# Optimization experiments

Measured on AMD Instinct MI355X. Metric: run time of the kernel, lower is better.

Reference implementation:

```python
import jax, jax.numpy as jnp
import numpy as np

N_NODES = 10000
N_EDGES = 640000
IN_CH, HID, OUT_CH = 128, 128, 64


def _gcn_conv(x, edge_index, edge_weight, W, b, n_nodes):
    # PyG GCNConv (default add_self_loops=True, normalize=True, bias=True):
    #   A_hat = A + I ; D = rowsum(A_hat) ; norm_e = D^-1/2[src] * w_e * D^-1/2[dst]
    #   out[dst] += norm_e * (x @ W)[src] ; out += b
    src, dst = edge_index[0], edge_index[1]
    loop = jnp.arange(n_nodes, dtype=edge_index.dtype)
    src = jnp.concatenate([src, loop])
    dst = jnp.concatenate([dst, loop])
    w = jnp.concatenate([edge_weight, jnp.ones((n_nodes,), edge_weight.dtype)])
    deg = jax.ops.segment_sum(w, dst, num_segments=n_nodes)  # scatter on col
    dinv = jnp.where(deg > 0, jax.lax.rsqrt(deg), 0.0).astype(x.dtype)
    norm = dinv[src] * w * dinv[dst]  # [E+N]
    xw = x @ W  # dense GEMM [N, out]
    msg = norm[:, None] * xw[src]  # gather + scale [E+N, out]
    out = jax.ops.segment_sum(msg, dst, num_segments=n_nodes)  # scatter-add
    return out + b


def setup_inputs() -> dict:
    key = jax.random.key(0)
    ks = jax.random.split(key, 8)
    x = jax.random.normal(ks[0], (N_NODES, IN_CH), dtype=jnp.float32)
    edge_index = jax.random.randint(ks[1], (2, N_EDGES), 0, N_NODES, dtype=jnp.int64)
    edge_weight = jax.random.uniform(ks[2], (N_EDGES,), dtype=jnp.float32)
    W1 = jax.random.normal(ks[3], (IN_CH, HID), dtype=jnp.float32) * 0.05
    b1 = jnp.zeros((HID,), jnp.float32)
    W2 = jax.random.normal(ks[4], (HID, OUT_CH), dtype=jnp.float32) * 0.05
    b2 = jnp.zeros((OUT_CH,), jnp.float32)
    return {"x": x, "edge_index": edge_index, "edge_weight": edge_weight,
            "W1": W1, "b1": b1, "W2": W2, "b2": b2}


def reference(x, edge_index, edge_weight, W1, b1, W2, b2):
    h = _gcn_conv(x, edge_index, edge_weight, W1, b1, N_NODES)
    h = jax.nn.relu(h)
    out = _gcn_conv(h, edge_index, edge_weight, W2, b2, N_NODES)
    return out
```

## Files before the change

kernel.cpp:

```cpp
#include <hip/hip_runtime.h>
#include <math.h>

#define N_NODES 10000
#define N_EDGES 640000
#define ELLW    192

#define CHUNKS  64
#define CHUNK_E 10000
#define GB      313

typedef unsigned long long ull;
typedef unsigned int uint;
typedef unsigned short ushort;
typedef unsigned char uchar;

#define FIXED_SCALE 262144.0f


__device__ __forceinline__ float bf_lo(uint u) { return __uint_as_float(u << 16); }
__device__ __forceinline__ float bf_hi(uint u) { return __uint_as_float(u & 0xffff0000u); }
__device__ __forceinline__ ushort f2bf(float v) {
    uint u = __float_as_uint(v);
    uint r = u + 0x7fffu + ((u >> 16) & 1u);
    return (ushort)(r >> 16);
}

__global__ __launch_bounds__(256) void kernelA(const int* __restrict__ ei,
                                               const float* __restrict__ ew,
                                               uint* __restrict__ sd32,
                                               uint* __restrict__ blockcnt,
                                               const float* __restrict__ x,
                                               const float* __restrict__ W1,
                                               ushort* __restrict__ xw1b) {
    __shared__ uint smem[N_NODES];
    const int tid = threadIdx.x;
    if (blockIdx.x < CHUNKS) {
        const int c = blockIdx.x;
        __shared__ int sflag;
        if (tid == 0) sflag = 0;
        for (int i = tid; i < N_NODES; i += 256) smem[i] = 0u;
        __syncthreads();
        int a = (tid < 64) ? ei[2 * (c * CHUNK_E + tid) + 1] : 0;
        if (a) atomicOr(&sflag, 1);
        __syncthreads();
        const int f = sflag;
        const ull* ei64 = (const ull*)ei;
        for (int k = tid; k < CHUNK_E; k += 256) {
            int e = c * CHUNK_E + k;
            int s, d;
            if (f) { s = ei[e];        d = ei[N_EDGES + e]; }
            else   { s = (int)ei64[e]; d = (int)ei64[N_EDGES + e]; }
            float w = ew[e];
            uint fx = (uint)(w * FIXED_SCALE + 0.5f);
            uint old = atomicAdd(&smem[d], (1u << 24) | fx);
            uint r = (old >> 24) & 15u;
            sd32[e] = (r << 28) | ((uint)d << 14) | (uint)s;
        }
        __syncthreads();
        for (int i = tid; i < N_NODES; i += 256)
            blockcnt[c * N_NODES + i] = smem[i];
    } else {
        constexpr int K = 128, TM = 32, KT = 32, NCOL = 128, RPT = 16;
        float* sA = (float*)smem;
        float* sB = sA + TM * (KT + 1);
        int blk = blockIdx.x - CHUNKS;
        int c = tid % NCOL, rr = tid / NCOL;
        int row0 = blk * TM;
        float acc[RPT];
#pragma unroll
        for (int r = 0; r < RPT; ++r) acc[r] = 0.0f;
        for (int k0 = 0; k0 < K; k0 += KT) {
            for (int i = tid; i < TM * KT; i += 256) {
                int r = i / KT, k = i % KT;
                int gr = row0 + r;
                sA[r * (KT + 1) + k] = (gr < N_NODES) ? x[gr * K + k0 + k] : 0.0f;
            }
            for (int i = tid; i < KT * NCOL; i += 256) {
                int k = i / NCOL, cc = i % NCOL;
                sB[k * NCOL + cc] = W1[(k0 + k) * NCOL + cc];
            }
            __syncthreads();
#pragma unroll
            for (int k = 0; k < KT; ++k) {
                float b = sB[k * NCOL + c];
#pragma unroll
                for (int r = 0; r < RPT; ++r)
                    acc[r] += sA[(rr * RPT + r) * (KT + 1) + k] * b;
            }
            __syncthreads();
        }
#pragma unroll
        for (int r = 0; r < RPT; ++r) {
            int gr = row0 + rr * RPT + r;
            if (gr < N_NODES) xw1b[gr * NCOL + c] = f2bf(acc[r]);
        }
    }
}

__global__ __launch_bounds__(256) void scanB(const uint* __restrict__ blockcnt,
                                             uchar* __restrict__ base8,
                                             int* __restrict__ cnt_arr,
                                             float* __restrict__ dinv) {
    int n = blockIdx.x * 256 + threadIdx.x;
    if (n >= N_NODES) return;
    uint wsum = 0;
    int run = 0;
#pragma unroll 8
    for (int c = 0; c < CHUNKS; ++c) {
        uint v = blockcnt[c * N_NODES + n];
        base8[c * N_NODES + n] = (uchar)run;
        run += (int)(v >> 24);
        wsum += v & 0xffffffu;
    }
    cnt_arr[n] = run;
    float dg = 1.0f + (float)wsum * (1.0f / FIXED_SCALE);
    dinv[n] = (float)(1.0 / sqrt((double)dg));
}

__global__ __launch_bounds__(256) void fillC(const uint* __restrict__ sd32,
                                             const float* __restrict__ ew,
                                             const uchar* __restrict__ base8,
                                             const float* __restrict__ dinv,
                                             ull* __restrict__ epack) {
    const int gid = blockIdx.x * 256 + threadIdx.x;
    const int stride = gridDim.x * 256;
    for (int e = gid; e < N_EDGES; e += stride) {
        uint sd = sd32[e];
        int s = (int)(sd & 0x3fffu);
        int d = (int)((sd >> 14) & 0x3fffu);
        int r = (int)(sd >> 28);
        int c = e / CHUNK_E;
        float nrm = dinv[s] * ew[e] * dinv[d];
        int slot = (int)base8[c * N_NODES + d] + r;
        if (slot < ELLW)
            epack[d * ELLW + slot] = ((ull)__float_as_uint(nrm) << 32) | (ull)(uint)s;
    }
}

__global__ __launch_bounds__(256) void aggC(const ushort* __restrict__ xw1b,
                                            const ull* __restrict__ epack,
                                            const int* __restrict__ cnt_arr,
                                            const float* __restrict__ dinv,
                                            const float* __restrict__ b1,
                                            const float* __restrict__ W2,
                                            ushort* __restrict__ xw2b) {
    __shared__ float hl[4][128];
    __shared__ float w2s[128 * 64];
    const uint* __restrict__ xw32 = (const uint*)xw1b;
    const int tid = threadIdx.x;
    int l = tid & 63;
    int wv = tid >> 6;
    int node = blockIdx.x * 4 + wv;

    for (int i = tid; i < 128 * 64; i += 256) w2s[i] = W2[i];

    int cnt = __builtin_amdgcn_readfirstlane(cnt_arr[node]);
    if (cnt > ELLW) cnt = ELLW;
    float dn = dinv[node];
    float d2 = dn * dn;
    uint su = xw32[node * 64 + l];
    float acc0 = d2 * bf_lo(su);
    float acc1 = d2 * bf_hi(su);
    const ull* ep = epack + (long)node * ELLW;
#pragma unroll 8
    for (int j = 0; j < cnt; ++j) {
        ull v = ep[j];
        uint s = (uint)v;
        float n = __uint_as_float((uint)(v >> 32));
        uint u = xw32[s * 64 + l];
        acc0 = fmaf(n, bf_lo(u), acc0);
        acc1 = fmaf(n, bf_hi(u), acc1);
    }
    float2 bb = ((const float2*)b1)[l];
    hl[wv][2 * l]     = fmaxf(acc0 + bb.x, 0.0f);
    hl[wv][2 * l + 1] = fmaxf(acc1 + bb.y, 0.0f);
    __syncthreads();

    float acc = 0.0f;
#pragma unroll 8
    for (int k = 0; k < 128; ++k)
        acc = fmaf(hl[wv][k], w2s[k * 64 + l], acc);
    xw2b[node * 64 + l] = f2bf(acc);
}

__global__ __launch_bounds__(256) void agg2(const ushort* __restrict__ xw2b,
                                            const ull* __restrict__ epack,
                                            const int* __restrict__ cnt_arr,
                                            const float* __restrict__ dinv,
                                            const float* __restrict__ b2,
                                            float* __restrict__ out) {
    const uint* __restrict__ xw32 = (const uint*)xw2b;
    int lane = threadIdx.x & 63;
    int half = lane >> 5;
    int q = lane & 31;
    int pair = blockIdx.x * 4 + (threadIdx.x >> 6);
    int A = pair * 2, B = A + 1;
    int cntA = __builtin_amdgcn_readfirstlane(cnt_arr[A]);
    int cntB = __builtin_amdgcn_readfirstlane(cnt_arr[B]);
    if (cntA > ELLW) cntA = ELLW;
    if (cntB > ELLW) cntB = ELLW;
    int myn = half ? B : A;
    int mycnt = half ? cntB : cntA;
    float dn = dinv[myn];
    float d2 = dn * dn;
    uint su = xw32[myn * 32 + q];
    float acc0 = d2 * bf_lo(su);
    float acc1 = d2 * bf_hi(su);
    const ull* epA = epack + (long)A * ELLW;
    const ull* epB = epack + (long)B * ELLW;
    int mx = cntA > cntB ? cntA : cntB;
#pragma unroll 4
    for (int j = 0; j < mx; ++j) {
        ull vA = epA[j];
        ull vB = epB[j];
        ull v = half ? vB : vA;
        uint s = (uint)v & 0xffffu;
        float n = (j < mycnt) ? __uint_as_float((uint)(v >> 32)) : 0.0f;
        uint u = xw32[s * 32 + q];
        acc0 = fmaf(n, bf_lo(u), acc0);
        acc1 = fmaf(n, bf_hi(u), acc1);
    }
    float2 bb = ((const float2*)b2)[q];
    float2 o;
    o.x = acc0 + bb.x;
    o.y = acc1 + bb.y;
    ((float2*)out)[myn * 32 + q] = o;
}

extern "C" void kernel_launch(void* const* d_in, const int* in_sizes, int n_in,
                              void* d_out, int out_size, void* d_ws, size_t ws_size,
                              hipStream_t stream) {
    const float* x  = (const float*)d_in[0];
    const int*   ei = (const int*)d_in[1];
    const float* ew = (const float*)d_in[2];
    const float* W1 = (const float*)d_in[3];
    const float* b1 = (const float*)d_in[4];
    const float* W2 = (const float*)d_in[5];
    const float* b2 = (const float*)d_in[6];
    float* out = (float*)d_out;

    char* ws = (char*)d_ws;
    ushort* xw1b    = (ushort*)(ws + 0);
    ushort* xw2b    = (ushort*)(ws + 5120000);
    ull*    epack   = (ull*)   (ws + 6400000);
    uint*   blockcnt= (uint*)  (ws + 21760000);
    uchar*  base8   = (uchar*) (ws + 26880000);
    uint*   sd32    = (uint*)  (ws + 28800000);
    int*    cnt_arr = (int*)   (ws + 31360000);
    float*  dinv    = (float*) (ws + 31400000);

    kernelA<<<CHUNKS + GB, 256, 0, stream>>>(ei, ew, sd32, blockcnt, x, W1, xw1b);
    scanB<<<(N_NODES + 255) / 256, 256, 0, stream>>>(blockcnt, base8, cnt_arr, dinv);
    fillC<<<512, 256, 0, stream>>>(sd32, ew, base8, dinv, epack);
    aggC<<<2500, 256, 0, stream>>>(xw1b, epack, cnt_arr, dinv, b1, W2, xw2b);
    agg2<<<1250, 256, 0, stream>>>(xw2b, epack, cnt_arr, dinv, b2, out);
}
```

Baseline: 166.4 us.

## Double edge chunks, shrink GEMM tile, pack W2 as bf16, vectorize ELL gathers

Doubles the number of edge-counting chunks, which halves edges per block, and halves the GEMM row tile so the launch has more, smaller blocks. In aggC, W2 is stored in shared memory as packed bf16 pairs, cutting LDS from 32KB to 16KB, and launch_bounds is raised to 8 blocks for higher occupancy. Both aggregation kernels now load ELL entries as 16-byte vectors and issue 8 independent gathers per iteration to raise memory-level parallelism. Rounding W2 to bf16 adds precision error, and the wider loads assume each row start in epack is 16-byte aligned.

```diff
diff --git a/kernel.cpp b/kernel.cpp
--- a/kernel.cpp
+++ b/kernel.cpp
@@ -5,9 +5,9 @@
 #define N_EDGES 640000
 #define ELLW    192
 
-#define CHUNKS  64
-#define CHUNK_E 10000
-#define GB      313
+#define CHUNKS  128
+#define CHUNK_E 5000
+#define GB      625
 
 typedef unsigned long long ull;
 typedef unsigned int uint;
@@ -60,7 +60,7 @@
         for (int i = tid; i < N_NODES; i += 256)
             blockcnt[c * N_NODES + i] = smem[i];
     } else {
-        constexpr int K = 128, TM = 32, KT = 32, NCOL = 128, RPT = 16;
+        constexpr int K = 128, TM = 16, KT = 32, NCOL = 128, RPT = 8;
         float* sA = (float*)smem;
         float* sB = sA + TM * (KT + 1);
         int blk = blockIdx.x - CHUNKS;
@@ -137,22 +137,27 @@
     }
 }
 
-__global__ __launch_bounds__(256) void aggC(const ushort* __restrict__ xw1b,
-                                            const ull* __restrict__ epack,
-                                            const int* __restrict__ cnt_arr,
-                                            const float* __restrict__ dinv,
-                                            const float* __restrict__ b1,
-                                            const float* __restrict__ W2,
-                                            ushort* __restrict__ xw2b) {
+__global__ __launch_bounds__(256, 8) void aggC(const ushort* __restrict__ xw1b,
+                                               const ull* __restrict__ epack,
+                                               const int* __restrict__ cnt_arr,
+                                               const float* __restrict__ dinv,
+                                               const float* __restrict__ b1,
+                                               const float* __restrict__ W2,
+                                               ushort* __restrict__ xw2b) {
     __shared__ float hl[4][128];
-    __shared__ float w2s[128 * 64];
+    __shared__ uint w2p[64 * 64];
     const uint* __restrict__ xw32 = (const uint*)xw1b;
     const int tid = threadIdx.x;
     int l = tid & 63;
     int wv = tid >> 6;
     int node = blockIdx.x * 4 + wv;
 
-    for (int i = tid; i < 128 * 64; i += 256) w2s[i] = W2[i];
+    for (int i = tid; i < 64 * 64; i += 256) {
+        int k2 = i >> 6, cc = i & 63;
+        uint lo = (uint)f2bf(W2[(2 * k2) * 64 + cc]);
+        uint hi = (uint)f2bf(W2[(2 * k2 + 1) * 64 + cc]);
+        w2p[i] = lo | (hi << 16);
+    }
 
     int cnt = __builtin_amdgcn_readfirstlane(cnt_arr[node]);
     if (cnt > ELLW) cnt = ELLW;
@@ -162,12 +167,50 @@
     float acc0 = d2 * bf_lo(su);
     float acc1 = d2 * bf_hi(su);
     const ull* ep = epack + (long)node * ELLW;
-#pragma unroll 8
-    for (int j = 0; j < cnt; ++j) {
+    int j = 0;
+    for (; j + 8 <= cnt; j += 8) {
+        ulonglong2 v0 = *(const ulonglong2*)(ep + j);
+        ulonglong2 v1 = *(const ulonglong2*)(ep + j + 2);
+        ulonglong2 v2 = *(const ulonglong2*)(ep + j + 4);
+        ulonglong2 v3 = *(const ulonglong2*)(ep + j + 6);
+        uint u0 = xw32[(uint)v0.x * 64 + l];
+        uint u1 = xw32[(uint)v0.y * 64 + l];
+        uint u2 = xw32[(uint)v1.x * 64 + l];
+        uint u3 = xw32[(uint)v1.y * 64 + l];
+        uint u4 = xw32[(uint)v2.x * 64 + l];
+        uint u5 = xw32[(uint)v2.y * 64 + l];
+        uint u6 = xw32[(uint)v3.x * 64 + l];
+        uint u7 = xw32[(uint)v3.y * 64 + l];
+        float n0 = __uint_as_float((uint)(v0.x >> 32));
+        float n1 = __uint_as_float((uint)(v0.y >> 32));
+        float n2 = __uint_as_float((uint)(v1.x >> 32));
+        float n3 = __uint_as_float((uint)(v1.y >> 32));
+        float n4 = __uint_as_float((uint)(v2.x >> 32));
+        float n5 = __uint_as_float((uint)(v2.y >> 32));
+        float n6 = __uint_as_float((uint)(v3.x >> 32));
+        float n7 = __uint_as_float((uint)(v3.y >> 32));
+        acc0 = fmaf(n0, bf_lo(u0), acc0); acc1 = fmaf(n0, bf_hi(u0), acc1);
+        acc0 = fmaf(n1, bf_lo(u1), acc0); acc1 = fmaf(n1, bf_hi(u1), acc1);
+        acc0 = fmaf(n2, bf_lo(u2), acc0); acc1 = fmaf(n2, bf_hi(u2), acc1);
+        acc0 = fmaf(n3, bf_lo(u3), acc0); acc1 = fmaf(n3, bf_hi(u3), acc1);
+        acc0 = fmaf(n4, bf_lo(u4), acc0); acc1 = fmaf(n4, bf_hi(u4), acc1);
+        acc0 = fmaf(n5, bf_lo(u5), acc0); acc1 = fmaf(n5, bf_hi(u5), acc1);
+        acc0 = fmaf(n6, bf_lo(u6), acc0); acc1 = fmaf(n6, bf_hi(u6), acc1);
+        acc0 = fmaf(n7, bf_lo(u7), acc0); acc1 = fmaf(n7, bf_hi(u7), acc1);
+    }
+    for (; j + 2 <= cnt; j += 2) {
+        ulonglong2 vv = *(const ulonglong2*)(ep + j);
+        uint u0 = xw32[(uint)vv.x * 64 + l];
+        uint u1 = xw32[(uint)vv.y * 64 + l];
+        float n0 = __uint_as_float((uint)(vv.x >> 32));
+        float n1 = __uint_as_float((uint)(vv.y >> 32));
+        acc0 = fmaf(n0, bf_lo(u0), acc0); acc1 = fmaf(n0, bf_hi(u0), acc1);
+        acc0 = fmaf(n1, bf_lo(u1), acc0); acc1 = fmaf(n1, bf_hi(u1), acc1);
+    }
+    if (j < cnt) {
         ull v = ep[j];
-        uint s = (uint)v;
+        uint u = xw32[(uint)v * 64 + l];
         float n = __uint_as_float((uint)(v >> 32));
-        uint u = xw32[s * 64 + l];
         acc0 = fmaf(n, bf_lo(u), acc0);
         acc1 = fmaf(n, bf_hi(u), acc1);
     }
@@ -178,8 +221,11 @@
 
     float acc = 0.0f;
 #pragma unroll 8
-    for (int k = 0; k < 128; ++k)
-        acc = fmaf(hl[wv][k], w2s[k * 64 + l], acc);
+    for (int k2 = 0; k2 < 64; ++k2) {
+        uint w = w2p[k2 * 64 + l];
+        acc = fmaf(hl[wv][2 * k2],     bf_lo(w), acc);
+        acc = fmaf(hl[wv][2 * k2 + 1], bf_hi(w), acc);
+    }
     xw2b[node * 64 + l] = f2bf(acc);
 }
 
@@ -209,10 +255,51 @@
     const ull* epA = epack + (long)A * ELLW;
     const ull* epB = epack + (long)B * ELLW;
     int mx = cntA > cntB ? cntA : cntB;
-#pragma unroll 4
-    for (int j = 0; j < mx; ++j) {
-        ull vA = epA[j];
-        ull vB = epB[j];
+    int j = 0;
+    for (; j + 8 <= mx; j += 8) {
+        ulonglong2 a0 = *(const ulonglong2*)(epA + j);
+        ulonglong2 a1 = *(const ulonglong2*)(epA + j + 2);
+        ulonglong2 a2 = *(const ulonglong2*)(epA + j + 4);
+        ulonglong2 a3 = *(const ulonglong2*)(epA + j + 6);
+        ulonglong2 b0 = *(const ulonglong2*)(epB + j);
+        ulonglong2 b1v = *(const ulonglong2*)(epB + j + 2);
+        ulonglong2 b2v = *(const ulonglong2*)(epB + j + 4);
+        ulonglong2 b3 = *(const ulonglong2*)(epB + j + 6);
+        ull e0 = half ? b0.x : a0.x;
+        ull e1 = half ? b0.y : a0.y;
+        ull e2 = half ? b1v.x : a1.x;
+        ull e3 = half ? b1v.y : a1.y;
+        ull e4 = half ? b2v.x : a2.x;
+        ull e5 = half ? b2v.y : a2.y;
+        ull e6 = half ? b3.x : a3.x;
+        ull e7 = half ? b3.y : a3.y;
+        uint u0 = xw32[((uint)e0 & 0xffffu) * 32 + q];
+        uint u1 = xw32[((uint)e1 & 0xffffu) * 32 + q];
+        uint u2 = xw32[((uint)e2 & 0xffffu) * 32 + q];
+        uint u3 = xw32[((uint)e3 & 0xffffu) * 32 + q];
+        uint u4 = xw32[((uint)e4 & 0xffffu) * 32 + q];
+        uint u5 = xw32[((uint)e5 & 0xffffu) * 32 + q];
+        uint u6 = xw32[((uint)e6 & 0xffffu) * 32 + q];
+        uint u7 = xw32[((uint)e7 & 0xffffu) * 32 + q];
+        float n0 = (j     < mycnt) ? __uint_as_float((uint)(e0 >> 32)) : 0.0f;
+        float n1 = (j + 1 < mycnt) ? __uint_as_float((uint)(e1 >> 32)) : 0.0f;
+        float n2 = (j + 2 < mycnt) ? __uint_as_float((uint)(e2 >> 32)) : 0.0f;
+        float n3 = (j + 3 < mycnt) ? __uint_as_float((uint)(e3 >> 32)) : 0.0f;
+        float n4 = (j + 4 < mycnt) ? __uint_as_float((uint)(e4 >> 32)) : 0.0f;
+        float n5 = (j + 5 < mycnt) ? __uint_as_float((uint)(e5 >> 32)) : 0.0f;
+        float n6 = (j + 6 < mycnt) ? __uint_as_float((uint)(e6 >> 32)) : 0.0f;
+        float n7 = (j + 7 < mycnt) ? __uint_as_float((uint)(e7 >> 32)) : 0.0f;
+        acc0 = fmaf(n0, bf_lo(u0), acc0); acc1 = fmaf(n0, bf_hi(u0), acc1);
+        acc0 = fmaf(n1, bf_lo(u1), acc0); acc1 = fmaf(n1, bf_hi(u1), acc1);
+        acc0 = fmaf(n2, bf_lo(u2), acc0); acc1 = fmaf(n2, bf_hi(u2), acc1);
+        acc0 = fmaf(n3, bf_lo(u3), acc0); acc1 = fmaf(n3, bf_hi(u3), acc1);
+        acc0 = fmaf(n4, bf_lo(u4), acc0); acc1 = fmaf(n4, bf_hi(u4), acc1);
+        acc0 = fmaf(n5, bf_lo(u5), acc0); acc1 = fmaf(n5, bf_hi(u5), acc1);
+        acc0 = fmaf(n6, bf_lo(u6), acc0); acc1 = fmaf(n6, bf_hi(u6), acc1);
+        acc0 = fmaf(n7, bf_lo(u7), acc0); acc1 = fmaf(n7, bf_hi(u7), acc1);
+    }
+    for (; j < mx; ++j) {
+        ull vA = epA[j], vB = epB[j];
         ull v = half ? vB : vA;
         uint s = (uint)v & 0xffffu;
         float n = (j < mycnt) ? __uint_as_float((uint)(v >> 32)) : 0.0f;
```

Result: faster. 159.3 us (-4.3%).
